# Kernel optimization log

Hardware: AMD Instinct MI355X
Metric: run time of the kernel (lower is better)

Reference implementation:

```python
import jax, jax.numpy as jnp
import numpy as np

# Rates 40MHz -> 60MHz => Fraction(1.5).limit_denominator(1000) = 3/2
UP, DOWN = 3, 2
MAX_RATE = max(UP, DOWN)
HALF_LEN = 10 * MAX_RATE                      # 30 (scipy.resample_poly default)
N_PRE_PAD = DOWN - (HALF_LEN % DOWN)          # 2
N_PRE_REMOVE = (HALF_LEN + N_PRE_PAD) // DOWN # 16
NUMTAPS_LS = 51
TAIL_ZEROS = 100
B, N = 8, 1048576


def _firwin_kaiser(numtaps, cutoff, beta):
    # scipy.signal.firwin(numtaps, cutoff, window=('kaiser', beta)), cutoff in Nyquist units
    m = np.arange(numtaps) - (numtaps - 1) / 2.0
    h = cutoff * np.sinc(cutoff * m)
    h *= np.kaiser(numtaps, beta)
    return h / h.sum()  # unit DC gain


def _band_int(k, f1, f2):
    # integral_{f1}^{f2} cos(pi*k*f) df, elementwise over integer array k
    k = np.asarray(k, dtype=float)
    safe = np.where(k == 0.0, 1.0, np.pi * k)
    return np.where(k == 0.0, f2 - f1, (np.sin(np.pi * k * f2) - np.sin(np.pi * k * f1)) / safe)


def _firls(numtaps, bands, desired):
    # Type-I linear-phase least-squares FIR (constant desired per band, unit weights)
    M = (numtaps - 1) // 2
    k = np.arange(M + 1)
    Q = np.zeros((M + 1, M + 1))
    rhs = np.zeros(M + 1)
    for f1, f2, d in zip(bands[0::2], bands[1::2], desired[0::2]):
        km = k[:, None] - k[None, :]
        kp = k[:, None] + k[None, :]
        Q += 0.5 * (_band_int(km, f1, f2) + _band_int(kp, f1, f2))
        rhs += d * _band_int(k, f1, f2)
    a = np.linalg.solve(Q, rhs)  # A(f) = sum_n a[n] cos(pi n f)
    half = a / 2.0
    half[0] = a[0]
    return np.concatenate([half[:0:-1], half])  # symmetric impulse response


def setup_inputs() -> dict:
    key = jax.random.key(0)
    x = jax.random.normal(key, (B, N), dtype=jnp.float32)
    # resample_poly anti-imaging filter, scaled by UP, with scipy's zero pre-padding
    h = _firwin_kaiser(2 * HALF_LEN + 1, 1.0 / MAX_RATE, 5.0) * UP
    h = np.concatenate([np.zeros(N_PRE_PAD), h])
    cutoff = DOWN / UP
    b = _firls(NUMTAPS_LS, [0.0, cutoff, cutoff + 0.1, 1.0], [1.0, 1.0, 0.0, 0.0])
    return {
        'x': x,
        'h_resample': jnp.asarray(h, jnp.float32),
        'b_fir': jnp.asarray(b, jnp.float32),
    }


def reference(x, h_resample, b_fir):
    b_sz, n = x.shape
    n_in = b_sz * n
    n_out = n_in * UP // DOWN + (1 if (n_in * UP) % DOWN else 0)
    xf = x.reshape(-1)
    Lh = h_resample.shape[0]
    # Fused polyphase resample: full convolution of UP-zero-stuffed signal
    # with h (flipped for true convolution), decimated by DOWN.
    y = jax.lax.conv_general_dilated(
        xf[None, None, :], h_resample[::-1][None, None, :],
        window_strides=(DOWN,), padding=[(Lh - 1, Lh - 1)],
        lhs_dilation=(UP,),
        dimension_numbers=('NCH', 'OIH', 'NCH'))[0, 0]
    u = y[N_PRE_REMOVE:N_PRE_REMOVE + n_out]               # == scipy.resample_poly
    up_padded = jnp.concatenate([u, jnp.zeros((TAIL_ZEROS,), x.dtype)])
    Lb = b_fir.shape[0]
    # lfilter(b, 1, .) == causal FIR: left-pad Lb-1 zeros, same-length output
    filt = jax.lax.conv_general_dilated(
        up_padded[None, None, :], b_fir[::-1][None, None, :],
        window_strides=(1,), padding=[(Lb - 1, 0)],
        dimension_numbers=('NCH', 'OIH', 'NCH'))[0, 0]
    total = n_out + TAIL_ZEROS
    per_b = total // b_sz
    return filt[:b_sz * per_b].reshape(b_sz, per_b)
```

## Files before the change

### kernel.cpp

```cpp
#include <hip/hip_runtime.h>


#define TPB 256
#define RPT 12
#define OTILE (TPB * RPT)
#define NCHUNK 528
#define NTAPS 55
#define CPSTRIDE 56

#define SLOT(c) ((c) ^ (((c) >> 3) & 7))

__global__ void build_coeffs(const float* __restrict__ h,
                             const float* __restrict__ b,
                             float* __restrict__ cp) {
    __shared__ float h_s[63];
    __shared__ float b_s[51];
    const int tid = threadIdx.x;
    if (tid < 63) h_s[tid] = h[tid];
    if (tid < 51) b_s[tid] = b[tid];
    __syncthreads();
    for (int idx = tid; idx < 3 * CPSTRIDE; idx += blockDim.x) {
        const int p = idx / CPSTRIDE;
        const int k = idx - p * CPSTRIDE;
        float acc = 0.0f;
        if (k < NTAPS) {
            const int j = p + 3 * k;
            for (int m = 0; m <= 50; ++m) {
                const int hi = j - 2 * m;
                if (hi >= 0 && hi <= 62) acc += b_s[m] * h_s[hi];
            }
        }
        cp[idx] = acc;
    }
}

__global__ __launch_bounds__(128) void boundary_fix(
    const float* __restrict__ x, const float* __restrict__ h,
    const float* __restrict__ b, float* __restrict__ out,
    int n_in, int n_out, int out_size)
{
    __shared__ float h_s[63];
    __shared__ float b_s[51];
    __shared__ float x_s[64];
    __shared__ float u_s[50];

    const int tid = threadIdx.x;
    if (tid < 63) h_s[tid] = h[tid];
    if (tid < 51) b_s[tid] = b[tid];

    if (blockIdx.x == 0) {
        if (tid < 44) x_s[tid] = (tid < n_in) ? x[tid] : 0.0f;
        __syncthreads();
        if (tid < 50) {
            const int s  = 2 * tid + 32;
            const int p0 = s % 3;
            const int q  = s / 3;
            float u = 0.0f;
            #pragma unroll
            for (int i = 0; i <= 20; ++i) {
                const int xi = q - i;
                u += h_s[p0 + 3 * i] * ((xi >= 0) ? x_s[xi] : 0.0f);
            }
            u_s[tid] = u;
        }
        __syncthreads();
        if (tid < 50) {
            float acc = 0.0f;
            for (int t = 0; t <= tid; ++t) acc += b_s[tid - t] * u_s[t];
            out[tid] = acc;
        }
    } else {
        const int t0   = n_out - 50;
        const int qmin = (2 * t0 + 32) / 3;
        const int xb   = qmin - 20;
        if (tid < 64) {
            const int xi = xb + tid;
            x_s[tid] = (xi >= 0 && xi < n_in) ? x[xi] : 0.0f;
        }
        __syncthreads();
        if (tid < 50) {
            const int t  = t0 + tid;
            const int s  = 2 * t + 32;
            const int p0 = s % 3;
            const int q  = s / 3;
            const int base = q - xb;
            float u = 0.0f;
            #pragma unroll
            for (int i = 0; i <= 20; ++i)
                u += h_s[p0 + 3 * i] * x_s[base - i];
            u_s[tid] = u;
        }
        __syncthreads();
        const int n_tail = out_size - n_out;
        if (tid < n_tail) {
            float acc = 0.0f;
            for (int j = tid; j <= 49; ++j) acc += b_s[tid + 50 - j] * u_s[j];
            out[n_out + tid] = acc;
        }
    }
}

#define GRP12(g, A, B, C, D) {                                          \
    const float4 q2 = c2q[g];                                           \
    const float4 q1 = c1q[g];                                           \
    const float4 q0 = c0q[g];                                           \
                                                               \
    a0  += q2.x * C.z;  a1  += q1.x * C.w;  a2  += q0.x * B.x;          \
    a3  += q2.x * B.x;  a4  += q1.x * B.y;  a5  += q0.x * B.z;          \
    a6  += q2.x * B.z;  a7  += q1.x * B.w;  a8  += q0.x * A.x;          \
    a9  += q2.x * A.x;  a10 += q1.x * A.y;  a11 += q0.x * A.z;          \
                                                               \
    a0  += q2.y * C.y;  a1  += q1.y * C.z;  a2  += q0.y * C.w;          \
    a3  += q2.y * C.w;  a4  += q1.y * B.x;  a5  += q0.y * B.y;          \
    a6  += q2.y * B.y;  a7  += q1.y * B.z;  a8  += q0.y * B.w;          \
    a9  += q2.y * B.w;  a10 += q1.y * A.x;  a11 += q0.y * A.y;          \
                                                               \
    a0  += q2.z * C.x;  a1  += q1.z * C.y;  a2  += q0.z * C.z;          \
    a3  += q2.z * C.z;  a4  += q1.z * C.w;  a5  += q0.z * B.x;          \
    a6  += q2.z * B.x;  a7  += q1.z * B.y;  a8  += q0.z * B.z;          \
    a9  += q2.z * B.z;  a10 += q1.z * B.w;  a11 += q0.z * A.x;          \
                                                               \
    a0  += q2.w * D.w;  a1  += q1.w * C.x;  a2  += q0.w * C.y;          \
    a3  += q2.w * C.y;  a4  += q1.w * C.z;  a5  += q0.w * C.w;          \
    a6  += q2.w * C.w;  a7  += q1.w * B.x;  a8  += q0.w * B.y;          \
    a9  += q2.w * B.y;  a10 += q1.w * B.z;  a11 += q0.w * B.w; }

#define GRP12T(g, A, B, C) {                                            \
    const float4 q2 = c2q[g];                                           \
    const float4 q1 = c1q[g];                                           \
    const float4 q0 = c0q[g];                                           \
    a0  += q2.x * C.z;  a1  += q1.x * C.w;  a2  += q0.x * B.x;          \
    a3  += q2.x * B.x;  a4  += q1.x * B.y;  a5  += q0.x * B.z;          \
    a6  += q2.x * B.z;  a7  += q1.x * B.w;  a8  += q0.x * A.x;          \
    a9  += q2.x * A.x;  a10 += q1.x * A.y;  a11 += q0.x * A.z;          \
    a0  += q2.y * C.y;  a1  += q1.y * C.z;  a2  += q0.y * C.w;          \
    a3  += q2.y * C.w;  a4  += q1.y * B.x;  a5  += q0.y * B.y;          \
    a6  += q2.y * B.y;  a7  += q1.y * B.z;  a8  += q0.y * B.w;          \
    a9  += q2.y * B.w;  a10 += q1.y * A.x;  a11 += q0.y * A.y;          \
    a0  += q2.z * C.x;  a1  += q1.z * C.y;  a2  += q0.z * C.z;          \
    a3  += q2.z * C.z;  a4  += q1.z * C.w;  a5  += q0.z * B.x;          \
    a6  += q2.z * B.x;  a7  += q1.z * B.y;  a8  += q0.z * B.z;          \
    a9  += q2.z * B.z;  a10 += q1.z * B.w;  a11 += q0.z * A.x; }

__global__ __launch_bounds__(TPB) void fused_fast(
    const float* __restrict__ x, const float* __restrict__ cp,
    float* __restrict__ out, int n_in, int n_out)
{
    __shared__ float4 xs4[NCHUNK];

    const int tid = threadIdx.x;
    const int bt  = blockIdx.x;
    const int o0  = bt * OTILE;
    const int n_tile0 = 2048 * bt - 44;

    const float4* c2q = (const float4*)(cp + 2 * CPSTRIDE);
    const float4* c1q = (const float4*)(cp + 1 * CPSTRIDE);
    const float4* c0q = (const float4*)(cp + 0 * CPSTRIDE);

    const bool interior = (n_tile0 >= 0) && (n_tile0 + 4 * NCHUNK <= n_in);
    if (interior) {
        const float4* gx = (const float4*)(x + n_tile0);
        const float4 g0 = gx[tid];
        const float4 g1 = gx[tid + 256];
        xs4[SLOT(tid)]       = g0;
        xs4[SLOT(tid + 256)] = g1;
        if (tid < NCHUNK - 512) {
            xs4[SLOT(tid + 512)] = gx[tid + 512];
        }
    } else {
        float* xsf = (float*)xs4;
        for (int i = tid; i < 4 * NCHUNK; i += TPB) {
            const int n = n_tile0 + i;
            const float v = (n >= 0 && n < n_in) ? x[n] : 0.0f;
            xsf[(SLOT(i >> 2) << 2) | (i & 3)] = v;
        }
    }
    __syncthreads();

    float a0 = 0.f, a1 = 0.f, a2 = 0.f, a3  = 0.f, a4  = 0.f, a5  = 0.f;
    float a6 = 0.f, a7 = 0.f, a8 = 0.f, a9  = 0.f, a10 = 0.f, a11 = 0.f;

    const int cbase = 2 * tid;
#define XS(j) xs4[SLOT(cbase + (j))]
    {
        float4 r0 = XS(15), r1 = XS(14), r2 = XS(13),
               r3 = XS(12), r4 = XS(11), r5 = XS(10);
        GRP12( 0, r0, r1, r2, r3);  r0 = XS(9);
        GRP12( 1, r1, r2, r3, r4);  r1 = XS(8);
        GRP12( 2, r2, r3, r4, r5);  r2 = XS(7);
        GRP12( 3, r3, r4, r5, r0);  r3 = XS(6);
        GRP12( 4, r4, r5, r0, r1);  r4 = XS(5);
        GRP12( 5, r5, r0, r1, r2);  r5 = XS(4);
        GRP12( 6, r0, r1, r2, r3);  r0 = XS(3);
        GRP12( 7, r1, r2, r3, r4);  r1 = XS(2);
        GRP12( 8, r2, r3, r4, r5);  r2 = XS(1);
        GRP12( 9, r3, r4, r5, r0);  r3 = XS(0);
        GRP12(10, r4, r5, r0, r1);
        GRP12(11, r5, r0, r1, r2);
        GRP12(12, r0, r1, r2, r3);
        GRP12T(13, r1, r2, r3);
    }
#undef XS

    const int ob = o0 + RPT * tid;
    if (ob >= 50 && ob + 11 < n_out) {
        float4* o4 = (float4*)(out + ob);
        o4[0] = make_float4(a0, a1, a2,  a3);
        o4[1] = make_float4(a4, a5, a6,  a7);
        o4[2] = make_float4(a8, a9, a10, a11);
    } else {
        const float accs[RPT] = {a0, a1, a2, a3, a4, a5, a6, a7, a8, a9, a10, a11};
#pragma unroll
        for (int d = 0; d < RPT; ++d) {
            const int o = ob + d;
            if (o >= 50 && o < n_out) out[o] = accs[d];
        }
    }
}

extern "C" void kernel_launch(void* const* d_in, const int* in_sizes, int n_in_arrs,
                              void* d_out, int out_size, void* d_ws, size_t ws_size,
                              hipStream_t stream) {
    const float* x = (const float*)d_in[0];
    const float* h = (const float*)d_in[1];
    const float* b = (const float*)d_in[2];
    float* out = (float*)d_out;
    float* cp  = (float*)d_ws;

    const int n_in  = in_sizes[0];
    const int n_out = (int)((long long)n_in * 3 / 2);

    build_coeffs<<<1, 64, 0, stream>>>(h, b, cp);

    const int nblocks = (n_out + OTILE - 1) / OTILE;
    fused_fast<<<nblocks, TPB, 0, stream>>>(x, cp, out, n_in, n_out);
    boundary_fix<<<2, 128, 0, stream>>>(x, h, b, out, n_in, n_out, out_size);
}
```

Measured before the change: 117.0 us.

## Fuse coefficient build, main FIR and boundary fix into one kernel

Merges the three kernel launches into a single launch. Each main block recomputes the 165 combined polyphase coefficients from h and b into shared memory, overlapping that with its global x loads. Two extra blocks at the end handle the head and tail boundary outputs. This removes launch overhead and the serial dependency on the coefficient-build kernel, at the cost of redundant per-block coefficient work and an extra barrier.

```diff
diff --git a/kernel.cpp b/kernel.cpp
--- a/kernel.cpp
+++ b/kernel.cpp
@@ -9,96 +9,6 @@
 #define CPSTRIDE 56
 
 #define SLOT(c) ((c) ^ (((c) >> 3) & 7))
-
-__global__ void build_coeffs(const float* __restrict__ h,
-                             const float* __restrict__ b,
-                             float* __restrict__ cp) {
-    __shared__ float h_s[63];
-    __shared__ float b_s[51];
-    const int tid = threadIdx.x;
-    if (tid < 63) h_s[tid] = h[tid];
-    if (tid < 51) b_s[tid] = b[tid];
-    __syncthreads();
-    for (int idx = tid; idx < 3 * CPSTRIDE; idx += blockDim.x) {
-        const int p = idx / CPSTRIDE;
-        const int k = idx - p * CPSTRIDE;
-        float acc = 0.0f;
-        if (k < NTAPS) {
-            const int j = p + 3 * k;
-            for (int m = 0; m <= 50; ++m) {
-                const int hi = j - 2 * m;
-                if (hi >= 0 && hi <= 62) acc += b_s[m] * h_s[hi];
-            }
-        }
-        cp[idx] = acc;
-    }
-}
-
-__global__ __launch_bounds__(128) void boundary_fix(
-    const float* __restrict__ x, const float* __restrict__ h,
-    const float* __restrict__ b, float* __restrict__ out,
-    int n_in, int n_out, int out_size)
-{
-    __shared__ float h_s[63];
-    __shared__ float b_s[51];
-    __shared__ float x_s[64];
-    __shared__ float u_s[50];
-
-    const int tid = threadIdx.x;
-    if (tid < 63) h_s[tid] = h[tid];
-    if (tid < 51) b_s[tid] = b[tid];
-
-    if (blockIdx.x == 0) {
-        if (tid < 44) x_s[tid] = (tid < n_in) ? x[tid] : 0.0f;
-        __syncthreads();
-        if (tid < 50) {
-            const int s  = 2 * tid + 32;
-            const int p0 = s % 3;
-            const int q  = s / 3;
-            float u = 0.0f;
-            #pragma unroll
-            for (int i = 0; i <= 20; ++i) {
-                const int xi = q - i;
-                u += h_s[p0 + 3 * i] * ((xi >= 0) ? x_s[xi] : 0.0f);
-            }
-            u_s[tid] = u;
-        }
-        __syncthreads();
-        if (tid < 50) {
-            float acc = 0.0f;
-            for (int t = 0; t <= tid; ++t) acc += b_s[tid - t] * u_s[t];
-            out[tid] = acc;
-        }
-    } else {
-        const int t0   = n_out - 50;
-        const int qmin = (2 * t0 + 32) / 3;
-        const int xb   = qmin - 20;
-        if (tid < 64) {
-            const int xi = xb + tid;
-            x_s[tid] = (xi >= 0 && xi < n_in) ? x[xi] : 0.0f;
-        }
-        __syncthreads();
-        if (tid < 50) {
-            const int t  = t0 + tid;
-            const int s  = 2 * t + 32;
-            const int p0 = s % 3;
-            const int q  = s / 3;
-            const int base = q - xb;
-            float u = 0.0f;
-            #pragma unroll
-            for (int i = 0; i <= 20; ++i)
-                u += h_s[p0 + 3 * i] * x_s[base - i];
-            u_s[tid] = u;
-        }
-        __syncthreads();
-        const int n_tail = out_size - n_out;
-        if (tid < n_tail) {
-            float acc = 0.0f;
-            for (int j = tid; j <= 49; ++j) acc += b_s[tid + 50 - j] * u_s[j];
-            out[n_out + tid] = acc;
-        }
-    }
-}
 
 #define GRP12(g, A, B, C, D) {                                          \
     const float4 q2 = c2q[g];                                           \
@@ -142,31 +52,115 @@
     a6  += q2.z * B.x;  a7  += q1.z * B.y;  a8  += q0.z * B.z;          \
     a9  += q2.z * B.z;  a10 += q1.z * B.w;  a11 += q0.z * A.x; }
 
-__global__ __launch_bounds__(TPB) void fused_fast(
-    const float* __restrict__ x, const float* __restrict__ cp,
-    float* __restrict__ out, int n_in, int n_out)
+__global__ __launch_bounds__(TPB) void fused_all(
+    const float* __restrict__ x, const float* __restrict__ h,
+    const float* __restrict__ b, float* __restrict__ out,
+    int n_in, int n_out, int out_size, int nmain)
 {
     __shared__ float4 xs4[NCHUNK];
+    __shared__ float4 cps4[3 * CPSTRIDE / 4];
+    __shared__ float  h_s[64];
+    __shared__ float  b_s[52];
 
     const int tid = threadIdx.x;
-    const int bt  = blockIdx.x;
-    const int o0  = bt * OTILE;
-    const int n_tile0 = 2048 * bt - 44;
-
-    const float4* c2q = (const float4*)(cp + 2 * CPSTRIDE);
-    const float4* c1q = (const float4*)(cp + 1 * CPSTRIDE);
-    const float4* c0q = (const float4*)(cp + 0 * CPSTRIDE);
+    const int bid = blockIdx.x;
+
+    float* const cps = (float*)cps4;
+
+    if (bid >= nmain) {
+        float* const x_s = (float*)xs4;
+        float* const u_s = ((float*)xs4) + 64;
+
+        if (tid < 63) h_s[tid] = h[tid];
+        if (tid < 51) b_s[tid] = b[tid];
+
+        if (bid == nmain) {
+            if (tid < 44) x_s[tid] = (tid < n_in) ? x[tid] : 0.0f;
+            __syncthreads();
+            if (tid < 50) {
+                const int s  = 2 * tid + 32;
+                const int p0 = s % 3;
+                const int q  = s / 3;
+                float u = 0.0f;
+                #pragma unroll
+                for (int i = 0; i <= 20; ++i) {
+                    const int xi = q - i;
+                    u += h_s[p0 + 3 * i] * ((xi >= 0) ? x_s[xi] : 0.0f);
+                }
+                u_s[tid] = u;
+            }
+            __syncthreads();
+            if (tid < 50) {
+                float acc = 0.0f;
+                for (int t = 0; t <= tid; ++t) acc += b_s[tid - t] * u_s[t];
+                out[tid] = acc;
+            }
+        } else {
+            const int t0   = n_out - 50;
+            const int qmin = (2 * t0 + 32) / 3;
+            const int xb   = qmin - 20;
+            if (tid < 64) {
+                const int xi = xb + tid;
+                x_s[tid] = (xi >= 0 && xi < n_in) ? x[xi] : 0.0f;
+            }
+            __syncthreads();
+            if (tid < 50) {
+                const int t  = t0 + tid;
+                const int s  = 2 * t + 32;
+                const int p0 = s % 3;
+                const int q  = s / 3;
+                const int base = q - xb;
+                float u = 0.0f;
+                #pragma unroll
+                for (int i = 0; i <= 20; ++i)
+                    u += h_s[p0 + 3 * i] * x_s[base - i];
+                u_s[tid] = u;
+            }
+            __syncthreads();
+            const int n_tail = out_size - n_out;
+            if (tid < n_tail) {
+                float acc = 0.0f;
+                for (int j = tid; j <= 49; ++j) acc += b_s[tid + 50 - j] * u_s[j];
+                out[n_out + tid] = acc;
+            }
+        }
+        return;
+    }
+
+    const int o0      = bid * OTILE;
+    const int n_tile0 = 2048 * bid - 44;
+
+    if (tid < 63) h_s[tid] = h[tid];
+    if (tid < 51) b_s[tid] = b[tid];
 
     const bool interior = (n_tile0 >= 0) && (n_tile0 + 4 * NCHUNK <= n_in);
+    float4 g0, g1, g2;
     if (interior) {
         const float4* gx = (const float4*)(x + n_tile0);
-        const float4 g0 = gx[tid];
-        const float4 g1 = gx[tid + 256];
+        g0 = gx[tid];
+        g1 = gx[tid + 256];
+        if (tid < NCHUNK - 512) g2 = gx[tid + 512];
+    }
+    __syncthreads();
+
+    if (tid < 3 * CPSTRIDE) {
+        const int p = tid / CPSTRIDE;
+        const int k = tid - p * CPSTRIDE;
+        float acc = 0.0f;
+        if (k < NTAPS) {
+            const int j  = p + 3 * k;
+            const int m0 = max(0, (j - 61) >> 1);
+            const int m1 = min(50, j >> 1);
+            for (int m = m0; m <= m1; ++m)
+                acc += b_s[m] * h_s[j - 2 * m];
+        }
+        cps[tid] = acc;
+    }
+
+    if (interior) {
         xs4[SLOT(tid)]       = g0;
         xs4[SLOT(tid + 256)] = g1;
-        if (tid < NCHUNK - 512) {
-            xs4[SLOT(tid + 512)] = gx[tid + 512];
-        }
+        if (tid < NCHUNK - 512) xs4[SLOT(tid + 512)] = g2;
     } else {
         float* xsf = (float*)xs4;
         for (int i = tid; i < 4 * NCHUNK; i += TPB) {
@@ -176,6 +170,10 @@
         }
     }
     __syncthreads();
+
+    const float4* c2q = cps4 + 2 * (CPSTRIDE / 4);
+    const float4* c1q = cps4 + 1 * (CPSTRIDE / 4);
+    const float4* c0q = cps4;
 
     float a0 = 0.f, a1 = 0.f, a2 = 0.f, a3  = 0.f, a4  = 0.f, a5  = 0.f;
     float a6 = 0.f, a7 = 0.f, a8 = 0.f, a9  = 0.f, a10 = 0.f, a11 = 0.f;
@@ -225,14 +223,11 @@
     const float* h = (const float*)d_in[1];
     const float* b = (const float*)d_in[2];
     float* out = (float*)d_out;
-    float* cp  = (float*)d_ws;
 
     const int n_in  = in_sizes[0];
     const int n_out = (int)((long long)n_in * 3 / 2);
 
-    build_coeffs<<<1, 64, 0, stream>>>(h, b, cp);
-
-    const int nblocks = (n_out + OTILE - 1) / OTILE;
-    fused_fast<<<nblocks, TPB, 0, stream>>>(x, cp, out, n_in, n_out);
-    boundary_fix<<<2, 128, 0, stream>>>(x, h, b, out, n_in, n_out, out_size);
+    const int nmain = (n_out + OTILE - 1) / OTILE;
+    fused_all<<<nmain + 2, TPB, 0, stream>>>(x, h, b, out,
+                                             n_in, n_out, out_size, nmain);
 }
```

Result: slower. 162.0 us (+38.5%).
